# Kernel optimization log

Measured on AMD Instinct MI355X. Metric: run time of the kernel, lower is better.

Reference implementation:

```python
import jax, jax.numpy as jnp
import numpy as np

MAXG = 8          # max adaptive sampling grid (boxes generated so ceil(roi_size) <= 8)
SCALE = 0.125     # spatial_scale / ds (ds = 1.0)


def setup_inputs() -> dict:
    key = jax.random.key(0)
    ks = jax.random.split(key, 12)
    bs, N, ch, H, W = 8, 128, 1280, 64, 64
    out_ch, inner = 1024, 5120
    z = jax.random.normal(ks[0], (bs, ch, H, W), jnp.float32)
    # boxes (x1, y1, x2, y2) in 512x512 image coords, sizes in [8, 64] px
    x1 = jax.random.uniform(ks[1], (bs, N), minval=0.0, maxval=448.0)
    y1 = jax.random.uniform(ks[2], (bs, N), minval=0.0, maxval=448.0)
    bw = jax.random.uniform(ks[3], (bs, N), minval=8.0, maxval=64.0)
    bh = jax.random.uniform(ks[4], (bs, N), minval=8.0, maxval=64.0)
    bboxes = jnp.stack([x1, y1, x1 + bw, y1 + bh], axis=-1)

    def lin(k, fan_in, shape):
        return jax.random.normal(k, shape, jnp.float32) * (1.0 / np.sqrt(fan_in))

    W1 = lin(ks[5], ch, (ch, inner)); b1 = jnp.zeros((inner,), jnp.float32)
    W2 = lin(ks[6], inner, (inner, out_ch)); b2 = jnp.zeros((out_ch,), jnp.float32)
    S1 = lin(ks[7], 2, (2, 64)); sb1 = jnp.zeros((64,), jnp.float32)
    S2 = lin(ks[8], 64, (64, 256)); sb2 = jnp.zeros((256,), jnp.float32)
    S3 = lin(ks[9], 256, (256, out_ch)); sb3 = jnp.zeros((out_ch,), jnp.float32)
    O = lin(ks[10], 2 * out_ch, (2 * out_ch, out_ch)); ob = jnp.zeros((out_ch,), jnp.float32)
    return dict(z=z, bboxes=bboxes, W1=W1, b1=b1, W2=W2, b2=b2,
                S1=S1, sb1=sb1, S2=S2, sb2=sb2, S3=S3, sb3=sb3, O=O, ob=ob)


def _prep(c, size):
    # torchvision bilinear border handling for one coordinate axis
    oob = (c < -1.0) | (c > size)
    cc = jnp.clip(c, 0.0, None)
    lo0 = jnp.floor(cc)
    hi_case = lo0 >= size - 1
    lo = jnp.minimum(lo0, size - 1).astype(jnp.int32)
    hi = jnp.minimum(lo0 + 1, size - 1).astype(jnp.int32)
    frac = jnp.where(hi_case, 0.0, cc - lo0)
    return lo, hi, frac, oob


def _roi_align_1x1(z, bboxes):
    # torchvision roi_align, output_size=1, aligned=True, sampling_ratio=-1
    bs, ch, H, W = z.shape
    N = bboxes.shape[1]
    boxes = jax.lax.stop_gradient(bboxes).reshape(-1, 4) * SCALE - 0.5  # aligned
    bidx = jnp.repeat(jnp.arange(bs), N)
    rw = boxes[:, 2] - boxes[:, 0]
    rh = boxes[:, 3] - boxes[:, 1]
    gw = jnp.clip(jnp.ceil(rw), 1, MAXG)   # adaptive grid: ceil(roi_size / 1)
    gh = jnp.clip(jnp.ceil(rh), 1, MAXG)
    count = gh * gw
    i = jnp.arange(MAXG, dtype=jnp.float32)
    ys = boxes[:, 1:2] + (i[None] + 0.5) * rh[:, None] / gh[:, None]  # [R, G]
    xs = boxes[:, 0:1] + (i[None] + 0.5) * rw[:, None] / gw[:, None]
    vy = i[None] < gh[:, None]
    vx = i[None] < gw[:, None]
    yl, yh, fy, oy = _prep(ys, H)
    xl, xh, fx, ox = _prep(xs, W)
    my = (vy & ~oy).astype(z.dtype)
    mx = (vx & ~ox).astype(z.dtype)
    mask = my[:, :, None] * mx[:, None, :]             # [R, G, G]
    hy, ly = 1.0 - fy, fy
    hx, lx = 1.0 - fx, fx
    zt = jnp.transpose(z, (0, 2, 3, 1))                # [bs, H, W, ch]
    acc = jnp.zeros((bs * N, ch), z.dtype)
    corners = [(yl, xl, hy, hx), (yl, xh, hy, lx), (yh, xl, ly, hx), (yh, xh, ly, lx)]
    for yi, xi, wy, wx in corners:
        wt = mask * (wy[:, :, None] * wx[:, None, :])  # [R, G, G]
        v = zt[bidx[:, None, None], yi[:, :, None], xi[:, None, :]]  # [R, G, G, ch]
        acc = acc + jnp.einsum('rgh,rghc->rc', wt, v)
    return (acc / count[:, None]).reshape(bs, N, ch)


def reference(z, bboxes, W1, b1, W2, b2, S1, sb1, S2, sb2, S3, sb3, O, ob):
    x = _roi_align_1x1(z, bboxes)                      # [bs, N, ch]
    x = jax.nn.relu(x @ W1 + b1) @ W2 + b2             # out MLP
    # BBoxSizeEmbedder: (h, w) = (y2 - y1, x2 - x1)
    sz = jnp.stack([bboxes[..., 3] - bboxes[..., 1],
                    bboxes[..., 2] - bboxes[..., 0]], axis=-1)
    e = jax.nn.relu(sz @ S1 + sb1)
    e = jax.nn.relu(e @ S2 + sb2)
    e = e @ S3 + sb3
    return jnp.concatenate([x, e], axis=-1) @ O + ob   # out2
```

## Files before the change

### kernel.cpp

```cpp
#include <hip/hip_runtime.h>

static constexpr int kBS    = 8;
static constexpr int kNROI  = 128;
static constexpr int kR     = kBS * kNROI;
static constexpr int kCH    = 1280;
static constexpr int kH     = 64;
static constexpr int kW     = 64;
static constexpr int kPIX   = kH * kW;
static constexpr int kINNER = 5120;
static constexpr int kOUTC  = 1024;
static constexpr int kXE    = 2 * kOUTC;
static constexpr int kE2    = 256;

typedef _Float16 half8 __attribute__((ext_vector_type(8)));
typedef float floatx4 __attribute__((ext_vector_type(4)));

__device__ __forceinline__ void gload_lds16(const _Float16* g, _Float16* l) {
    __builtin_amdgcn_global_load_lds(
        (const __attribute__((address_space(1))) void*)g,
        (__attribute__((address_space(3))) void*)l,
        16, 0, 0);
}

__global__ __launch_bounds__(256) void transpose_z_f16(const float* __restrict__ z,
                                                       _Float16* __restrict__ zt) {
    __shared__ float tile[64][33];
    const int b  = blockIdx.z;
    const int p0 = blockIdx.x * 32;
    const int c0 = blockIdx.y * 64;
    const int tx = threadIdx.x;
    const int ty = threadIdx.y;
    const float* zb = z + (size_t)b * kCH * kPIX;
    _Float16* ztb = zt + (size_t)b * kPIX * kCH;
#pragma unroll
    for (int i = 0; i < 8; ++i) {
        const int cl = ty + i * 8;
        tile[cl][tx] = zb[(size_t)(c0 + cl) * kPIX + p0 + tx];
    }
    __syncthreads();
#pragma unroll
    for (int i = 0; i < 4; ++i) {
        const int pl = ty + i * 8;
        union { _Float16 h[2]; unsigned int u; } pk;
        pk.h[0] = (_Float16)tile[2 * tx][pl];
        pk.h[1] = (_Float16)tile[2 * tx + 1][pl];
        *(unsigned int*)(ztb + (size_t)(p0 + pl) * kCH + c0 + 2 * tx) = pk.u;
    }
}

struct RoiLists {
    int   yidx[16], xidx[16];
    float ywt[16], xwt[16];
    int   ny, nx;
    float invCount;
};

__device__ inline void build_lists(const float* __restrict__ bboxes, int r, RoiLists* L) {
    const float x1 = bboxes[r * 4 + 0] * 0.125f - 0.5f;
    const float y1 = bboxes[r * 4 + 1] * 0.125f - 0.5f;
    const float x2 = bboxes[r * 4 + 2] * 0.125f - 0.5f;
    const float y2 = bboxes[r * 4 + 3] * 0.125f - 0.5f;
    const float rw = x2 - x1, rh = y2 - y1;
    const float gwf = fminf(fmaxf(ceilf(rw), 1.0f), 8.0f);
    const float ghf = fminf(fmaxf(ceilf(rh), 1.0f), 8.0f);
    const int gw = (int)gwf, gh = (int)ghf;
    L->invCount = 1.0f / (gwf * ghf);
    for (int g = 0; g < gh; ++g) {
        const float c   = y1 + ((float)g + 0.5f) * rh / ghf;
        const bool oob  = (c < -1.0f) || (c > 64.0f);
        const float cc  = fmaxf(c, 0.0f);
        const float lo0 = floorf(cc);
        const bool hic  = (lo0 >= 63.0f);
        const int lo    = (int)fminf(lo0, 63.0f);
        const int hi    = (int)fminf(lo0 + 1.0f, 63.0f);
        const float fr  = hic ? 0.0f : (cc - lo0);
        const float m   = oob ? 0.0f : 1.0f;
        L->yidx[2 * g]     = lo; L->ywt[2 * g]     = m * (1.0f - fr);
        L->yidx[2 * g + 1] = hi; L->ywt[2 * g + 1] = m * fr;
    }
    L->ny = 2 * gh;
    for (int g = 0; g < gw; ++g) {
        const float c   = x1 + ((float)g + 0.5f) * rw / gwf;
        const bool oob  = (c < -1.0f) || (c > 64.0f);
        const float cc  = fmaxf(c, 0.0f);
        const float lo0 = floorf(cc);
        const bool hic  = (lo0 >= 63.0f);
        const int lo    = (int)fminf(lo0, 63.0f);
        const int hi    = (int)fminf(lo0 + 1.0f, 63.0f);
        const float fr  = hic ? 0.0f : (cc - lo0);
        const float m   = oob ? 0.0f : 1.0f;
        L->xidx[2 * g]     = lo; L->xwt[2 * g]     = m * (1.0f - fr);
        L->xidx[2 * g + 1] = hi; L->xwt[2 * g + 1] = m * fr;
    }
    L->nx = 2 * gw;
}

__global__ __launch_bounds__(256) void roi_gather_f16_v2(const _Float16* __restrict__ zt,
                                                         const float* __restrict__ bboxes,
                                                         _Float16* __restrict__ x) {
    const int r  = blockIdx.y;
    const int b  = r >> 7;
    const int cg = blockIdx.x * 32;
    const int t  = threadIdx.x;
    __shared__ RoiLists L;
    __shared__ int   off[256];
    __shared__ float wt[256];
    __shared__ float accs[8][32][9];
    if (t == 0) build_lists(bboxes, r, &L);
    __syncthreads();
    const int np = L.ny * L.nx;
    if (t < np) {
        const int iy = t / L.nx;
        const int ix = t - iy * L.nx;
        off[t] = (L.yidx[iy] * kW + L.xidx[ix]) * kCH;
        wt[t]  = L.ywt[iy] * L.xwt[ix];
    }
    __syncthreads();
    const int lc = t & 31;
    const int pg = t >> 5;
    const _Float16* base = zt + (size_t)b * kPIX * kCH + (size_t)(cg + lc) * 8;
    float a[8] = {0.f, 0.f, 0.f, 0.f, 0.f, 0.f, 0.f, 0.f};
    for (int p = pg; p < np; p += 8) {
        const float w = wt[p];
        const half8 v = *(const half8*)(base + off[p]);
#pragma unroll
        for (int q = 0; q < 8; ++q) a[q] += w * (float)v[q];
    }
#pragma unroll
    for (int q = 0; q < 8; ++q) accs[pg][lc][q] = a[q];
    __syncthreads();
    const int rc = t >> 3, ch = t & 7;
    float s = 0.f;
#pragma unroll
    for (int g = 0; g < 8; ++g) s += accs[g][rc][ch];
    x[(size_t)r * kCH + (size_t)(cg + rc) * 8 + ch] = (_Float16)(s * L.invCount);
}

__global__ __launch_bounds__(256) void roi_gather_direct(const float* __restrict__ z,
                                                         const float* __restrict__ bboxes,
                                                         _Float16* __restrict__ x) {
    const int r = blockIdx.x;
    const int b = r >> 7;
    __shared__ RoiLists L;
    if (threadIdx.x == 0) build_lists(bboxes, r, &L);
    __syncthreads();
    const int ny = L.ny, nx = L.nx;
    const float ic = L.invCount;
    const float* zb = z + (size_t)b * kCH * kPIX;
    for (int c = threadIdx.x; c < kCH; c += 256) {
        const float* zc = zb + (size_t)c * kPIX;
        float acc = 0.f;
        for (int iy = 0; iy < ny; ++iy) {
            const float wy = L.ywt[iy];
            const int base = L.yidx[iy] * kW;
            for (int ix = 0; ix < nx; ++ix)
                acc += wy * L.xwt[ix] * zc[base + L.xidx[ix]];
        }
        x[(size_t)r * kCH + c] = (_Float16)(acc * ic);
    }
}

__global__ __launch_bounds__(256) void convert_transpose(const float* __restrict__ W,
                                                         _Float16* __restrict__ Wt,
                                                         int K, int N) {
    __shared__ float tile[32][33];
    const int n0 = blockIdx.x * 32;
    const int k0 = blockIdx.y * 32;
    const int tx = threadIdx.x;
    const int ty = threadIdx.y;
#pragma unroll
    for (int i = 0; i < 4; ++i)
        tile[ty + i * 8][tx] = W[(size_t)(k0 + ty + i * 8) * N + n0 + tx];
    __syncthreads();
#pragma unroll
    for (int i = 0; i < 4; ++i)
        Wt[(size_t)(n0 + ty + i * 8) * K + k0 + tx] = (_Float16)tile[tx][ty + i * 8];
}

template <int NSPLIT, bool FUSED, bool RELU, bool F16OUT>
__global__ __launch_bounds__(256) void gemm_f16(const _Float16* __restrict__ A,
                                                const _Float16* __restrict__ Bt,
                                                const float* __restrict__ bias,
                                                void* __restrict__ Out,
                                                int Kfull, int ldc) {
    __shared__ _Float16 As[2][128 * 32];
    __shared__ _Float16 Bs[2][128 * 32];
    const int t    = threadIdx.x;
    const int lane = t & 63;
    const int wave = t >> 6;
    const int m0 = blockIdx.y * 128, n0 = blockIdx.x * 128;
    const int Ksplit = Kfull / NSPLIT;
    const int s  = FUSED ? 0 : blockIdx.z;
    const int Nn = gridDim.x * 128;
    const int Mm = gridDim.y * 128;

    const int c0 = t, c1 = t + 256;
    const _Float16* Ag0 = A + (size_t)(m0 + (c0 >> 2)) * Kfull + (c0 & 3) * 8 + s * Ksplit;
    const _Float16* Ag1 = A + (size_t)(m0 + (c1 >> 2)) * Kfull + (c1 & 3) * 8 + s * Ksplit;
    const _Float16* Bg0 = Bt + (size_t)(n0 + (c0 >> 2)) * Kfull + (c0 & 3) * 8 + s * Ksplit;
    const _Float16* Bg1 = Bt + (size_t)(n0 + (c1 >> 2)) * Kfull + (c1 & 3) * 8 + s * Ksplit;

    const int wm = (wave >> 1) * 64;
    const int wn = (wave & 1) * 64;
    const int fm = lane & 15;
    const int kq = (lane >> 4) * 8;

    floatx4 acc[4][4];
#pragma unroll
    for (int i = 0; i < 4; ++i)
#pragma unroll
        for (int j = 0; j < 4; ++j) acc[i][j] = (floatx4){0.f, 0.f, 0.f, 0.f};

    const int nsteps = Ksplit / 32;

    gload_lds16(Ag0, &As[0][c0 * 8]);
    gload_lds16(Ag1, &As[0][c1 * 8]);
    gload_lds16(Bg0, &Bs[0][c0 * 8]);
    gload_lds16(Bg1, &Bs[0][c1 * 8]);
    __syncthreads();

    for (int ks = 0; ks < nsteps; ++ks) {
        const int cur = ks & 1;
        if (ks + 1 < nsteps) {
            const int kn = (ks + 1) * 32;
            gload_lds16(Ag0 + kn, &As[cur ^ 1][c0 * 8]);
            gload_lds16(Ag1 + kn, &As[cur ^ 1][c1 * 8]);
            gload_lds16(Bg0 + kn, &Bs[cur ^ 1][c0 * 8]);
            gload_lds16(Bg1 + kn, &Bs[cur ^ 1][c1 * 8]);
        }
        half8 af[4], bfv[4];
#pragma unroll
        for (int i = 0; i < 4; ++i)
            af[i] = *(const half8*)&As[cur][(wm + i * 16 + fm) * 32 + kq];
#pragma unroll
        for (int j = 0; j < 4; ++j)
            bfv[j] = *(const half8*)&Bs[cur][(wn + j * 16 + fm) * 32 + kq];
#pragma unroll
        for (int i = 0; i < 4; ++i)
#pragma unroll
            for (int j = 0; j < 4; ++j)
                acc[i][j] = __builtin_amdgcn_mfma_f32_16x16x32_f16(af[i], bfv[j], acc[i][j], 0, 0, 0);
        __syncthreads();
    }

    const int qr = (lane >> 4) * 4;
    if (FUSED) {
#pragma unroll
        for (int j = 0; j < 4; ++j) {
            const int col = n0 + wn + j * 16 + fm;
            const float bv = bias[col];
#pragma unroll
            for (int i = 0; i < 4; ++i) {
                const int row = m0 + wm + i * 16 + qr;
#pragma unroll
                for (int rr = 0; rr < 4; ++rr) {
                    float v = acc[i][j][rr] + bv;
                    if (RELU) v = fmaxf(v, 0.f);
                    if (F16OUT)
                        ((_Float16*)Out)[(size_t)(row + rr) * ldc + col] = (_Float16)v;
                    else
                        ((float*)Out)[(size_t)(row + rr) * ldc + col] = v;
                }
            }
        }
    } else {
        float* Pp = (float*)Out + (size_t)s * Mm * Nn;
#pragma unroll
        for (int j = 0; j < 4; ++j) {
            const int col = n0 + wn + j * 16 + fm;
#pragma unroll
            for (int i = 0; i < 4; ++i) {
                const int row = m0 + wm + i * 16 + qr;
#pragma unroll
                for (int rr = 0; rr < 4; ++rr)
                    Pp[(size_t)(row + rr) * Nn + col] = acc[i][j][rr];
            }
        }
    }
}

template <bool RELU, bool F16OUT, int NSPLIT>
__global__ __launch_bounds__(256) void reduce_splitk(const float* __restrict__ P,
                                                     const float* __restrict__ bias,
                                                     void* __restrict__ Cout,
                                                     int Nn, int ldc) {
    const size_t idx = ((size_t)blockIdx.x * 256 + threadIdx.x) * 4;
    const size_t MN  = (size_t)gridDim.x * 1024;
    const int m = (int)(idx / (size_t)Nn);
    const int n = (int)(idx % (size_t)Nn);
    float4 acc = *(const float4*)(P + idx);
#pragma unroll
    for (int s = 1; s < NSPLIT; ++s) {
        const float4 v = *(const float4*)(P + (size_t)s * MN + idx);
        acc.x += v.x; acc.y += v.y; acc.z += v.z; acc.w += v.w;
    }
    const float4 b4 = *(const float4*)(bias + n);
    acc.x += b4.x; acc.y += b4.y; acc.z += b4.z; acc.w += b4.w;
    if (RELU) {
        acc.x = fmaxf(acc.x, 0.f); acc.y = fmaxf(acc.y, 0.f);
        acc.z = fmaxf(acc.z, 0.f); acc.w = fmaxf(acc.w, 0.f);
    }
    if (F16OUT) {
        union { _Float16 h[4]; uint2 u; } pk;
        pk.h[0] = (_Float16)acc.x; pk.h[1] = (_Float16)acc.y;
        pk.h[2] = (_Float16)acc.z; pk.h[3] = (_Float16)acc.w;
        *(uint2*)((_Float16*)Cout + (size_t)m * ldc + n) = pk.u;
    } else {
        *(float4*)((float*)Cout + (size_t)m * ldc + n) = acc;
    }
}

__global__ __launch_bounds__(256) void size_mlp12(const float* __restrict__ bboxes,
                                                  const float* __restrict__ S1,
                                                  const float* __restrict__ sb1,
                                                  const float* __restrict__ S2,
                                                  const float* __restrict__ sb2,
                                                  _Float16* __restrict__ h2out) {
    const int r0 = blockIdx.x * 4;
    const int t  = threadIdx.x;
    __shared__ float sz[4][2];
    __shared__ float h1[4][64];
    if (t < 8) {
        const int row = t >> 1;
        const int c   = t & 1;
        const float* bb = bboxes + (size_t)(r0 + row) * 4;
        sz[row][c] = (c == 0) ? (bb[3] - bb[1]) : (bb[2] - bb[0]);
    }
    __syncthreads();
    {
        const int row = t >> 6;
        const int j   = t & 63;
        const float v = sz[row][0] * S1[j] + sz[row][1] * S1[64 + j] + sb1[j];
        h1[row][j] = fmaxf(v, 0.0f);
    }
    __syncthreads();
    {
        float acc[4];
        const float b = sb2[t];
#pragma unroll
        for (int row = 0; row < 4; ++row) acc[row] = b;
#pragma unroll 16
        for (int k = 0; k < 64; ++k) {
            const float w = S2[k * 256 + t];
#pragma unroll
            for (int row = 0; row < 4; ++row) acc[row] += h1[row][k] * w;
        }
#pragma unroll
        for (int row = 0; row < 4; ++row)
            h2out[(size_t)(r0 + row) * kE2 + t] = (_Float16)fmaxf(acc[row], 0.0f);
    }
}

extern "C" void kernel_launch(void* const* d_in, const int* in_sizes, int n_in,
                              void* d_out, int out_size, void* d_ws, size_t ws_size,
                              hipStream_t stream) {
    (void)in_sizes; (void)n_in; (void)out_size;
    const float* z   = (const float*)d_in[0];
    const float* bb  = (const float*)d_in[1];
    const float* W1  = (const float*)d_in[2];
    const float* b1  = (const float*)d_in[3];
    const float* W2  = (const float*)d_in[4];
    const float* b2  = (const float*)d_in[5];
    const float* S1  = (const float*)d_in[6];
    const float* sb1 = (const float*)d_in[7];
    const float* S2  = (const float*)d_in[8];
    const float* sb2 = (const float*)d_in[9];
    const float* S3  = (const float*)d_in[10];
    const float* sb3 = (const float*)d_in[11];
    const float* O   = (const float*)d_in[12];
    const float* ob  = (const float*)d_in[13];
    float* out = (float*)d_out;

    char* ws = (char*)d_ws;
    size_t off = 0;
    auto alloc = [&](size_t bytes) {
        void* p = ws + off;
        off += (bytes + 255) & ~(size_t)255;
        return p;
    };
    _Float16* x    = (_Float16*)alloc((size_t)kR * kCH * 2);
    _Float16* h    = (_Float16*)alloc((size_t)kR * kINNER * 2);
    _Float16* xe   = (_Float16*)alloc((size_t)kR * kXE * 2);
    _Float16* W1t  = (_Float16*)alloc((size_t)kINNER * kCH * 2);
    _Float16* W2t  = (_Float16*)alloc((size_t)kOUTC * kINNER * 2);
    _Float16* Ot   = (_Float16*)alloc((size_t)kOUTC * kXE * 2);
    _Float16* S3t  = (_Float16*)alloc((size_t)kOUTC * kE2 * 2);
    _Float16* h2f  = (_Float16*)alloc((size_t)kR * kE2 * 2);
    float*    P    = (float*)alloc((size_t)2 * kR * kINNER * 4);
    const size_t ztBytes = (size_t)kBS * kPIX * kCH * 2;
    _Float16* zt  = (_Float16*)(ws + off);
    const bool useT = (off + ztBytes) <= ws_size;

    hipLaunchKernelGGL(convert_transpose, dim3(kINNER / 32, kCH / 32), dim3(32, 8), 0, stream,
                       W1, W1t, kCH, kINNER);
    hipLaunchKernelGGL(convert_transpose, dim3(kOUTC / 32, kINNER / 32), dim3(32, 8), 0, stream,
                       W2, W2t, kINNER, kOUTC);
    hipLaunchKernelGGL(convert_transpose, dim3(kOUTC / 32, kXE / 32), dim3(32, 8), 0, stream,
                       O, Ot, kXE, kOUTC);
    hipLaunchKernelGGL(convert_transpose, dim3(kOUTC / 32, kE2 / 32), dim3(32, 8), 0, stream,
                       S3, S3t, kE2, kOUTC);

    if (useT) {
        hipLaunchKernelGGL(transpose_z_f16, dim3(kPIX / 32, kCH / 64, kBS), dim3(32, 8), 0,
                           stream, z, zt);
        hipLaunchKernelGGL(roi_gather_f16_v2, dim3(kCH / 256, kR), dim3(256), 0, stream,
                           zt, bb, x);
    } else {
        hipLaunchKernelGGL(roi_gather_direct, dim3(kR), dim3(256), 0, stream, z, bb, x);
    }

    hipLaunchKernelGGL(size_mlp12, dim3(kR / 4), dim3(256), 0, stream,
                       bb, S1, sb1, S2, sb2, h2f);
    hipLaunchKernelGGL((gemm_f16<4, false, false, false>),
                       dim3(kOUTC / 128, kR / 128, 4), dim3(256), 0, stream,
                       h2f, S3t, nullptr, P, kE2, 0);
    hipLaunchKernelGGL((reduce_splitk<false, true, 4>),
                       dim3((size_t)kR * kOUTC / 1024), dim3(256), 0, stream,
                       P, sb3, xe + kOUTC, kOUTC, kXE);

    hipLaunchKernelGGL((gemm_f16<2, false, false, false>),
                       dim3(kINNER / 128, kR / 128, 2), dim3(256), 0, stream,
                       x, W1t, nullptr, P, kCH, 0);
    hipLaunchKernelGGL((reduce_splitk<true, true, 2>),
                       dim3((size_t)kR * kINNER / 1024), dim3(256), 0, stream,
                       P, b1, h, kINNER, kINNER);

    hipLaunchKernelGGL((gemm_f16<4, false, false, false>),
                       dim3(kOUTC / 128, kR / 128, 4), dim3(256), 0, stream,
                       h, W2t, nullptr, P, kINNER, 0);
    hipLaunchKernelGGL((reduce_splitk<false, true, 4>),
                       dim3((size_t)kR * kOUTC / 1024), dim3(256), 0, stream,
                       P, b2, xe, kOUTC, kXE);

    hipLaunchKernelGGL((gemm_f16<4, false, false, false>),
                       dim3(kOUTC / 128, kR / 128, 4), dim3(256), 0, stream,
                       xe, Ot, nullptr, P, kXE, 0);
    hipLaunchKernelGGL((reduce_splitk<false, false, 4>),
                       dim3((size_t)kR * kOUTC / 1024), dim3(256), 0, stream,
                       P, ob, out, kOUTC, kOUTC);
}
```

Baseline: 458.8 us.

## Replace split-K GEMMs with fused-epilogue tiles and merge weight conversions

Removes the split-K partial buffer and the separate reduce kernels. Each GEMM now computes its full K range and applies bias, ReLU and fp16 conversion in the epilogue. Small-N GEMMs use 64x64 tiles to keep enough blocks in flight. The four weight convert-transpose launches are merged into one kernel indexed by block ID. This cuts fp32 partial-sum traffic and launch count, at the cost of fewer, longer-running blocks with lower per-block parallelism along K.

```diff
diff --git a/kernel.cpp b/kernel.cpp
--- a/kernel.cpp
+++ b/kernel.cpp
@@ -160,153 +160,114 @@
     }
 }
 
-__global__ __launch_bounds__(256) void convert_transpose(const float* __restrict__ W,
-                                                         _Float16* __restrict__ Wt,
-                                                         int K, int N) {
-    __shared__ float tile[32][33];
-    const int n0 = blockIdx.x * 32;
-    const int k0 = blockIdx.y * 32;
+__global__ __launch_bounds__(256) void convert_all(const float* __restrict__ W1,
+                                                   const float* __restrict__ W2,
+                                                   const float* __restrict__ O,
+                                                   const float* __restrict__ S3,
+                                                   _Float16* __restrict__ W1t,
+                                                   _Float16* __restrict__ W2t,
+                                                   _Float16* __restrict__ Ot,
+                                                   _Float16* __restrict__ S3t) {
+    const int bid = blockIdx.x;
+    const float* W; _Float16* Wt; int K, N, tile;
+    if (bid < 6400)        { W = W1; Wt = W1t; K = kCH;    N = kINNER; tile = bid; }
+    else if (bid < 11520)  { W = W2; Wt = W2t; K = kINNER; N = kOUTC;  tile = bid - 6400; }
+    else if (bid < 13568)  { W = O;  Wt = Ot;  K = kXE;    N = kOUTC;  tile = bid - 11520; }
+    else                   { W = S3; Wt = S3t; K = kE2;    N = kOUTC;  tile = bid - 13568; }
+    const int nt = N / 32;
+    const int n0 = (tile % nt) * 32;
+    const int k0 = (tile / nt) * 32;
+    __shared__ float tilebuf[32][33];
     const int tx = threadIdx.x;
     const int ty = threadIdx.y;
 #pragma unroll
     for (int i = 0; i < 4; ++i)
-        tile[ty + i * 8][tx] = W[(size_t)(k0 + ty + i * 8) * N + n0 + tx];
+        tilebuf[ty + i * 8][tx] = W[(size_t)(k0 + ty + i * 8) * N + n0 + tx];
     __syncthreads();
 #pragma unroll
     for (int i = 0; i < 4; ++i)
-        Wt[(size_t)(n0 + ty + i * 8) * K + k0 + tx] = (_Float16)tile[tx][ty + i * 8];
-}
-
-template <int NSPLIT, bool FUSED, bool RELU, bool F16OUT>
-__global__ __launch_bounds__(256) void gemm_f16(const _Float16* __restrict__ A,
-                                                const _Float16* __restrict__ Bt,
-                                                const float* __restrict__ bias,
-                                                void* __restrict__ Out,
-                                                int Kfull, int ldc) {
-    __shared__ _Float16 As[2][128 * 32];
-    __shared__ _Float16 Bs[2][128 * 32];
+        Wt[(size_t)(n0 + ty + i * 8) * K + k0 + tx] = (_Float16)tilebuf[tx][ty + i * 8];
+}
+
+template <int BM, int BN, bool RELU, bool F16OUT>
+__global__ __launch_bounds__(256) void gemm_fused(const _Float16* __restrict__ A,
+                                                  const _Float16* __restrict__ Bt,
+                                                  const float* __restrict__ bias,
+                                                  void* __restrict__ Out,
+                                                  int Kfull, int ldc) {
+    constexpr int ACH = BM * 4;
+    constexpr int BCH = BN * 4;
+    constexpr int FI  = BM / 32;
+    constexpr int FJ  = BN / 32;
+    __shared__ _Float16 As[2][BM * 32];
+    __shared__ _Float16 Bs[2][BN * 32];
     const int t    = threadIdx.x;
     const int lane = t & 63;
     const int wave = t >> 6;
-    const int m0 = blockIdx.y * 128, n0 = blockIdx.x * 128;
-    const int Ksplit = Kfull / NSPLIT;
-    const int s  = FUSED ? 0 : blockIdx.z;
-    const int Nn = gridDim.x * 128;
-    const int Mm = gridDim.y * 128;
-
-    const int c0 = t, c1 = t + 256;
-    const _Float16* Ag0 = A + (size_t)(m0 + (c0 >> 2)) * Kfull + (c0 & 3) * 8 + s * Ksplit;
-    const _Float16* Ag1 = A + (size_t)(m0 + (c1 >> 2)) * Kfull + (c1 & 3) * 8 + s * Ksplit;
-    const _Float16* Bg0 = Bt + (size_t)(n0 + (c0 >> 2)) * Kfull + (c0 & 3) * 8 + s * Ksplit;
-    const _Float16* Bg1 = Bt + (size_t)(n0 + (c1 >> 2)) * Kfull + (c1 & 3) * 8 + s * Ksplit;
-
-    const int wm = (wave >> 1) * 64;
-    const int wn = (wave & 1) * 64;
+    const int m0 = blockIdx.y * BM, n0 = blockIdx.x * BN;
+
+    const int wm = (wave >> 1) * (BM / 2);
+    const int wn = (wave & 1) * (BN / 2);
     const int fm = lane & 15;
     const int kq = (lane >> 4) * 8;
 
-    floatx4 acc[4][4];
-#pragma unroll
-    for (int i = 0; i < 4; ++i)
-#pragma unroll
-        for (int j = 0; j < 4; ++j) acc[i][j] = (floatx4){0.f, 0.f, 0.f, 0.f};
-
-    const int nsteps = Ksplit / 32;
-
-    gload_lds16(Ag0, &As[0][c0 * 8]);
-    gload_lds16(Ag1, &As[0][c1 * 8]);
-    gload_lds16(Bg0, &Bs[0][c0 * 8]);
-    gload_lds16(Bg1, &Bs[0][c1 * 8]);
+    auto stage = [&](int buf, int kk) {
+#pragma unroll
+        for (int cc = t; cc < ACH; cc += 256)
+            gload_lds16(A + (size_t)(m0 + (cc >> 2)) * Kfull + (cc & 3) * 8 + kk,
+                        &As[buf][cc * 8]);
+#pragma unroll
+        for (int cc = t; cc < BCH; cc += 256)
+            gload_lds16(Bt + (size_t)(n0 + (cc >> 2)) * Kfull + (cc & 3) * 8 + kk,
+                        &Bs[buf][cc * 8]);
+    };
+
+    floatx4 acc[FI][FJ];
+#pragma unroll
+    for (int i = 0; i < FI; ++i)
+#pragma unroll
+        for (int j = 0; j < FJ; ++j) acc[i][j] = (floatx4){0.f, 0.f, 0.f, 0.f};
+
+    const int nsteps = Kfull / 32;
+    stage(0, 0);
     __syncthreads();
 
     for (int ks = 0; ks < nsteps; ++ks) {
         const int cur = ks & 1;
-        if (ks + 1 < nsteps) {
-            const int kn = (ks + 1) * 32;
-            gload_lds16(Ag0 + kn, &As[cur ^ 1][c0 * 8]);
-            gload_lds16(Ag1 + kn, &As[cur ^ 1][c1 * 8]);
-            gload_lds16(Bg0 + kn, &Bs[cur ^ 1][c0 * 8]);
-            gload_lds16(Bg1 + kn, &Bs[cur ^ 1][c1 * 8]);
-        }
-        half8 af[4], bfv[4];
-#pragma unroll
-        for (int i = 0; i < 4; ++i)
+        if (ks + 1 < nsteps) stage(cur ^ 1, (ks + 1) * 32);
+        half8 af[FI], bfv[FJ];
+#pragma unroll
+        for (int i = 0; i < FI; ++i)
             af[i] = *(const half8*)&As[cur][(wm + i * 16 + fm) * 32 + kq];
 #pragma unroll
-        for (int j = 0; j < 4; ++j)
+        for (int j = 0; j < FJ; ++j)
             bfv[j] = *(const half8*)&Bs[cur][(wn + j * 16 + fm) * 32 + kq];
 #pragma unroll
-        for (int i = 0; i < 4; ++i)
-#pragma unroll
-            for (int j = 0; j < 4; ++j)
+        for (int i = 0; i < FI; ++i)
+#pragma unroll
+            for (int j = 0; j < FJ; ++j)
                 acc[i][j] = __builtin_amdgcn_mfma_f32_16x16x32_f16(af[i], bfv[j], acc[i][j], 0, 0, 0);
         __syncthreads();
     }
 
     const int qr = (lane >> 4) * 4;
-    if (FUSED) {
-#pragma unroll
-        for (int j = 0; j < 4; ++j) {
-            const int col = n0 + wn + j * 16 + fm;
-            const float bv = bias[col];
-#pragma unroll
-            for (int i = 0; i < 4; ++i) {
-                const int row = m0 + wm + i * 16 + qr;
-#pragma unroll
-                for (int rr = 0; rr < 4; ++rr) {
-                    float v = acc[i][j][rr] + bv;
-                    if (RELU) v = fmaxf(v, 0.f);
-                    if (F16OUT)
-                        ((_Float16*)Out)[(size_t)(row + rr) * ldc + col] = (_Float16)v;
-                    else
-                        ((float*)Out)[(size_t)(row + rr) * ldc + col] = v;
-                }
+#pragma unroll
+    for (int j = 0; j < FJ; ++j) {
+        const int col = n0 + wn + j * 16 + fm;
+        const float bv = bias[col];
+#pragma unroll
+        for (int i = 0; i < FI; ++i) {
+            const int row = m0 + wm + i * 16 + qr;
+#pragma unroll
+            for (int rr = 0; rr < 4; ++rr) {
+                float v = acc[i][j][rr] + bv;
+                if (RELU) v = fmaxf(v, 0.f);
+                if (F16OUT)
+                    ((_Float16*)Out)[(size_t)(row + rr) * ldc + col] = (_Float16)v;
+                else
+                    ((float*)Out)[(size_t)(row + rr) * ldc + col] = v;
             }
         }
-    } else {
-        float* Pp = (float*)Out + (size_t)s * Mm * Nn;
-#pragma unroll
-        for (int j = 0; j < 4; ++j) {
-            const int col = n0 + wn + j * 16 + fm;
-#pragma unroll
-            for (int i = 0; i < 4; ++i) {
-                const int row = m0 + wm + i * 16 + qr;
-#pragma unroll
-                for (int rr = 0; rr < 4; ++rr)
-                    Pp[(size_t)(row + rr) * Nn + col] = acc[i][j][rr];
-            }
-        }
-    }
-}
-
-template <bool RELU, bool F16OUT, int NSPLIT>
-__global__ __launch_bounds__(256) void reduce_splitk(const float* __restrict__ P,
-                                                     const float* __restrict__ bias,
-                                                     void* __restrict__ Cout,
-                                                     int Nn, int ldc) {
-    const size_t idx = ((size_t)blockIdx.x * 256 + threadIdx.x) * 4;
-    const size_t MN  = (size_t)gridDim.x * 1024;
-    const int m = (int)(idx / (size_t)Nn);
-    const int n = (int)(idx % (size_t)Nn);
-    float4 acc = *(const float4*)(P + idx);
-#pragma unroll
-    for (int s = 1; s < NSPLIT; ++s) {
-        const float4 v = *(const float4*)(P + (size_t)s * MN + idx);
-        acc.x += v.x; acc.y += v.y; acc.z += v.z; acc.w += v.w;
-    }
-    const float4 b4 = *(const float4*)(bias + n);
-    acc.x += b4.x; acc.y += b4.y; acc.z += b4.z; acc.w += b4.w;
-    if (RELU) {
-        acc.x = fmaxf(acc.x, 0.f); acc.y = fmaxf(acc.y, 0.f);
-        acc.z = fmaxf(acc.z, 0.f); acc.w = fmaxf(acc.w, 0.f);
-    }
-    if (F16OUT) {
-        union { _Float16 h[4]; uint2 u; } pk;
-        pk.h[0] = (_Float16)acc.x; pk.h[1] = (_Float16)acc.y;
-        pk.h[2] = (_Float16)acc.z; pk.h[3] = (_Float16)acc.w;
-        *(uint2*)((_Float16*)Cout + (size_t)m * ldc + n) = pk.u;
-    } else {
-        *(float4*)((float*)Cout + (size_t)m * ldc + n) = acc;
     }
 }
 
@@ -386,19 +347,12 @@
     _Float16* Ot   = (_Float16*)alloc((size_t)kOUTC * kXE * 2);
     _Float16* S3t  = (_Float16*)alloc((size_t)kOUTC * kE2 * 2);
     _Float16* h2f  = (_Float16*)alloc((size_t)kR * kE2 * 2);
-    float*    P    = (float*)alloc((size_t)2 * kR * kINNER * 4);
     const size_t ztBytes = (size_t)kBS * kPIX * kCH * 2;
     _Float16* zt  = (_Float16*)(ws + off);
     const bool useT = (off + ztBytes) <= ws_size;
 
-    hipLaunchKernelGGL(convert_transpose, dim3(kINNER / 32, kCH / 32), dim3(32, 8), 0, stream,
-                       W1, W1t, kCH, kINNER);
-    hipLaunchKernelGGL(convert_transpose, dim3(kOUTC / 32, kINNER / 32), dim3(32, 8), 0, stream,
-                       W2, W2t, kINNER, kOUTC);
-    hipLaunchKernelGGL(convert_transpose, dim3(kOUTC / 32, kXE / 32), dim3(32, 8), 0, stream,
-                       O, Ot, kXE, kOUTC);
-    hipLaunchKernelGGL(convert_transpose, dim3(kOUTC / 32, kE2 / 32), dim3(32, 8), 0, stream,
-                       S3, S3t, kE2, kOUTC);
+    hipLaunchKernelGGL(convert_all, dim3(13824), dim3(32, 8), 0, stream,
+                       W1, W2, O, S3, W1t, W2t, Ot, S3t);
 
     if (useT) {
         hipLaunchKernelGGL(transpose_z_f16, dim3(kPIX / 32, kCH / 64, kBS), dim3(32, 8), 0,
@@ -411,31 +365,19 @@
 
     hipLaunchKernelGGL(size_mlp12, dim3(kR / 4), dim3(256), 0, stream,
                        bb, S1, sb1, S2, sb2, h2f);
-    hipLaunchKernelGGL((gemm_f16<4, false, false, false>),
-                       dim3(kOUTC / 128, kR / 128, 4), dim3(256), 0, stream,
-                       h2f, S3t, nullptr, P, kE2, 0);
-    hipLaunchKernelGGL((reduce_splitk<false, true, 4>),
-                       dim3((size_t)kR * kOUTC / 1024), dim3(256), 0, stream,
-                       P, sb3, xe + kOUTC, kOUTC, kXE);
-
-    hipLaunchKernelGGL((gemm_f16<2, false, false, false>),
-                       dim3(kINNER / 128, kR / 128, 2), dim3(256), 0, stream,
-                       x, W1t, nullptr, P, kCH, 0);
-    hipLaunchKernelGGL((reduce_splitk<true, true, 2>),
-                       dim3((size_t)kR * kINNER / 1024), dim3(256), 0, stream,
-                       P, b1, h, kINNER, kINNER);
-
-    hipLaunchKernelGGL((gemm_f16<4, false, false, false>),
-                       dim3(kOUTC / 128, kR / 128, 4), dim3(256), 0, stream,
-                       h, W2t, nullptr, P, kINNER, 0);
-    hipLaunchKernelGGL((reduce_splitk<false, true, 4>),
-                       dim3((size_t)kR * kOUTC / 1024), dim3(256), 0, stream,
-                       P, b2, xe, kOUTC, kXE);
-
-    hipLaunchKernelGGL((gemm_f16<4, false, false, false>),
-                       dim3(kOUTC / 128, kR / 128, 4), dim3(256), 0, stream,
-                       xe, Ot, nullptr, P, kXE, 0);
-    hipLaunchKernelGGL((reduce_splitk<false, false, 4>),
-                       dim3((size_t)kR * kOUTC / 1024), dim3(256), 0, stream,
-                       P, ob, out, kOUTC, kOUTC);
-}
+    hipLaunchKernelGGL((gemm_fused<64, 64, false, true>),
+                       dim3(kOUTC / 64, kR / 64), dim3(256), 0, stream,
+                       h2f, S3t, sb3, xe + kOUTC, kE2, kXE);
+
+    hipLaunchKernelGGL((gemm_fused<128, 128, true, true>),
+                       dim3(kINNER / 128, kR / 128), dim3(256), 0, stream,
+                       x, W1t, b1, h, kCH, kINNER);
+
+    hipLaunchKernelGGL((gemm_fused<64, 64, false, true>),
+                       dim3(kOUTC / 64, kR / 64), dim3(256), 0, stream,
+                       h, W2t, b2, xe, kINNER, kXE);
+
+    hipLaunchKernelGGL((gemm_fused<64, 64, false, false>),
+                       dim3(kOUTC / 64, kR / 64), dim3(256), 0, stream,
+                       xe, Ot, ob, out, kXE, kOUTC);
+}
```

Measured after the change: 494.3 us. 7.7% more time.

## Merge weight conversions into one launch, fuse GEMM epilogues, raise split-K

Applied to the files above, without the earlier changes.

The four weight convert/transpose launches become a single kernel that picks its matrix from the block index. The S3 and W1 GEMMs now run unsplit, with bias, ReLU and f16 output fused into the epilogue, so their split-K partial writes and reduce kernels go away. The W2 and O GEMMs move from split-K 4 to 8 to raise occupancy on the small 1024-wide outputs, at the cost of more partial-sum traffic in the reduce. The workspace buffer for partial sums is resized to match.

```diff
diff --git a/kernel.cpp b/kernel.cpp
--- a/kernel.cpp
+++ b/kernel.cpp
@@ -160,21 +160,33 @@
     }
 }
 
-__global__ __launch_bounds__(256) void convert_transpose(const float* __restrict__ W,
-                                                         _Float16* __restrict__ Wt,
-                                                         int K, int N) {
-    __shared__ float tile[32][33];
-    const int n0 = blockIdx.x * 32;
-    const int k0 = blockIdx.y * 32;
+__global__ __launch_bounds__(256) void convert_all(const float* __restrict__ W1,
+                                                   const float* __restrict__ W2,
+                                                   const float* __restrict__ O,
+                                                   const float* __restrict__ S3,
+                                                   _Float16* __restrict__ W1t,
+                                                   _Float16* __restrict__ W2t,
+                                                   _Float16* __restrict__ Ot,
+                                                   _Float16* __restrict__ S3t) {
+    const int bid = blockIdx.x;
+    const float* W; _Float16* Wt; int K, N, tile;
+    if (bid < 6400)        { W = W1; Wt = W1t; K = kCH;    N = kINNER; tile = bid; }
+    else if (bid < 11520)  { W = W2; Wt = W2t; K = kINNER; N = kOUTC;  tile = bid - 6400; }
+    else if (bid < 13568)  { W = O;  Wt = Ot;  K = kXE;    N = kOUTC;  tile = bid - 11520; }
+    else                   { W = S3; Wt = S3t; K = kE2;    N = kOUTC;  tile = bid - 13568; }
+    const int nt = N / 32;
+    const int n0 = (tile % nt) * 32;
+    const int k0 = (tile / nt) * 32;
+    __shared__ float tilebuf[32][33];
     const int tx = threadIdx.x;
     const int ty = threadIdx.y;
 #pragma unroll
     for (int i = 0; i < 4; ++i)
-        tile[ty + i * 8][tx] = W[(size_t)(k0 + ty + i * 8) * N + n0 + tx];
+        tilebuf[ty + i * 8][tx] = W[(size_t)(k0 + ty + i * 8) * N + n0 + tx];
     __syncthreads();
 #pragma unroll
     for (int i = 0; i < 4; ++i)
-        Wt[(size_t)(n0 + ty + i * 8) * K + k0 + tx] = (_Float16)tile[tx][ty + i * 8];
+        Wt[(size_t)(n0 + ty + i * 8) * K + k0 + tx] = (_Float16)tilebuf[tx][ty + i * 8];
 }
 
 template <int NSPLIT, bool FUSED, bool RELU, bool F16OUT>
@@ -386,19 +398,13 @@
     _Float16* Ot   = (_Float16*)alloc((size_t)kOUTC * kXE * 2);
     _Float16* S3t  = (_Float16*)alloc((size_t)kOUTC * kE2 * 2);
     _Float16* h2f  = (_Float16*)alloc((size_t)kR * kE2 * 2);
-    float*    P    = (float*)alloc((size_t)2 * kR * kINNER * 4);
+    float*    P    = (float*)alloc((size_t)8 * kR * kOUTC * 4);
     const size_t ztBytes = (size_t)kBS * kPIX * kCH * 2;
     _Float16* zt  = (_Float16*)(ws + off);
     const bool useT = (off + ztBytes) <= ws_size;
 
-    hipLaunchKernelGGL(convert_transpose, dim3(kINNER / 32, kCH / 32), dim3(32, 8), 0, stream,
-                       W1, W1t, kCH, kINNER);
-    hipLaunchKernelGGL(convert_transpose, dim3(kOUTC / 32, kINNER / 32), dim3(32, 8), 0, stream,
-                       W2, W2t, kINNER, kOUTC);
-    hipLaunchKernelGGL(convert_transpose, dim3(kOUTC / 32, kXE / 32), dim3(32, 8), 0, stream,
-                       O, Ot, kXE, kOUTC);
-    hipLaunchKernelGGL(convert_transpose, dim3(kOUTC / 32, kE2 / 32), dim3(32, 8), 0, stream,
-                       S3, S3t, kE2, kOUTC);
+    hipLaunchKernelGGL(convert_all, dim3(13824), dim3(32, 8), 0, stream,
+                       W1, W2, O, S3, W1t, W2t, Ot, S3t);
 
     if (useT) {
         hipLaunchKernelGGL(transpose_z_f16, dim3(kPIX / 32, kCH / 64, kBS), dim3(32, 8), 0,
@@ -411,31 +417,25 @@
 
     hipLaunchKernelGGL(size_mlp12, dim3(kR / 4), dim3(256), 0, stream,
                        bb, S1, sb1, S2, sb2, h2f);
-    hipLaunchKernelGGL((gemm_f16<4, false, false, false>),
-                       dim3(kOUTC / 128, kR / 128, 4), dim3(256), 0, stream,
-                       h2f, S3t, nullptr, P, kE2, 0);
-    hipLaunchKernelGGL((reduce_splitk<false, true, 4>),
-                       dim3((size_t)kR * kOUTC / 1024), dim3(256), 0, stream,
-                       P, sb3, xe + kOUTC, kOUTC, kXE);
-
-    hipLaunchKernelGGL((gemm_f16<2, false, false, false>),
-                       dim3(kINNER / 128, kR / 128, 2), dim3(256), 0, stream,
-                       x, W1t, nullptr, P, kCH, 0);
-    hipLaunchKernelGGL((reduce_splitk<true, true, 2>),
-                       dim3((size_t)kR * kINNER / 1024), dim3(256), 0, stream,
-                       P, b1, h, kINNER, kINNER);
-
-    hipLaunchKernelGGL((gemm_f16<4, false, false, false>),
-                       dim3(kOUTC / 128, kR / 128, 4), dim3(256), 0, stream,
+    hipLaunchKernelGGL((gemm_f16<1, true, false, true>),
+                       dim3(kOUTC / 128, kR / 128), dim3(256), 0, stream,
+                       h2f, S3t, sb3, xe + kOUTC, kE2, kXE);
+
+    hipLaunchKernelGGL((gemm_f16<1, true, true, true>),
+                       dim3(kINNER / 128, kR / 128), dim3(256), 0, stream,
+                       x, W1t, b1, h, kCH, kINNER);
+
+    hipLaunchKernelGGL((gemm_f16<8, false, false, false>),
+                       dim3(kOUTC / 128, kR / 128, 8), dim3(256), 0, stream,
                        h, W2t, nullptr, P, kINNER, 0);
-    hipLaunchKernelGGL((reduce_splitk<false, true, 4>),
+    hipLaunchKernelGGL((reduce_splitk<false, true, 8>),
                        dim3((size_t)kR * kOUTC / 1024), dim3(256), 0, stream,
                        P, b2, xe, kOUTC, kXE);
 
-    hipLaunchKernelGGL((gemm_f16<4, false, false, false>),
-                       dim3(kOUTC / 128, kR / 128, 4), dim3(256), 0, stream,
+    hipLaunchKernelGGL((gemm_f16<8, false, false, false>),
+                       dim3(kOUTC / 128, kR / 128, 8), dim3(256), 0, stream,
                        xe, Ot, nullptr, P, kXE, 0);
-    hipLaunchKernelGGL((reduce_splitk<false, false, 4>),
+    hipLaunchKernelGGL((reduce_splitk<false, false, 8>),
                        dim3((size_t)kR * kOUTC / 1024), dim3(256), 0, stream,
                        P, ob, out, kOUTC, kOUTC);
 }
```

Measured after the change: 440.0 us. 1.04x faster.
